# Performance work log

Measured on AMD Instinct MI355X. Metric: run time of the kernel, lower is better.

## Reference

```python
import jax, jax.numpy as jnp
import numpy as np

B, C, H, W = 16, 256, 64, 64
K = 1024


def setup_inputs() -> dict:
    key = jax.random.key(0)
    k1, k2 = jax.random.split(key)
    z = jax.random.normal(k1, (B, C, H, W), dtype=jnp.float32)
    codebook = jax.random.normal(k2, (K, C), dtype=jnp.float32)
    return {"z": z, "codebook": codebook}


def reference(z, codebook):
    # assign: nearest-code indices via squared euclidean distance
    b, c, h, w = z.shape
    zf = jnp.transpose(z, (0, 2, 3, 1)).reshape(-1, c)            # [N, C]
    # ||z||^2 - 2 z.cb^T + ||cb||^2  -> [N, K]
    dists = (jnp.sum(zf * zf, axis=1, keepdims=True)
             - 2.0 * jnp.einsum('nc,kc->nk', zf, codebook)
             + jnp.sum(codebook * codebook, axis=1)[None, :])
    idx = jnp.argmin(dists, axis=1)                                # [N]
    indices = idx.reshape(b, 1, h, w)                              # [B,1,H,W]
    # embed_code: gather codebook rows, back to BCHW
    zq = codebook[idx].reshape(b, h, w, c)                         # [B,H,W,C]
    zq = jnp.transpose(zq, (0, 3, 1, 2))                           # [B,C,H,W]
    return zq, indices
```

## Files before the change

kernel.cpp:

```cpp
#include <hip/hip_runtime.h>


#define HWSZ 4096
#define CDIM 256
#define KCODES 1024
#define NPIX 65536
#define ZQ_ELEMS (16 * 256 * 4096)
#define MARGIN 0.75f

#define WS_CBSWZ 0
#define WS_CBN64 524288
#define WS_CBN32 532480
#define WS_CNT   536576
#define WS_LISTS 536592

#define L_NRM    65536
#define L_MK     69632
#define L_SBEST  72704
#define L_FLP    73216
#define L_FLQ    73728
#define L_LCNT   74240
#define L_TOTAL  74496

typedef __attribute__((ext_vector_type(8))) short bf16x8;
typedef __attribute__((ext_vector_type(4))) float f32x4;
typedef __attribute__((ext_vector_type(4))) unsigned short us4;

#define MFMA16(a, b, c) __builtin_amdgcn_mfma_f32_16x16x32_bf16(a, b, c, 0, 0, 0)

__device__ __forceinline__ unsigned short f2bf(float f) {
  unsigned u = __float_as_uint(f);
  unsigned r = u + 0x7FFFu + ((u >> 16) & 1u);
  return (unsigned short)(r >> 16);
}

__device__ __forceinline__ unsigned cvtpk(float lo, float hi) {
  unsigned r;
  asm("v_cvt_pk_bf16_f32 %0, %1, %2" : "=v"(r) : "v"(lo), "v"(hi));
  return r;
}

__device__ __forceinline__ void gload_lds16(const void* g, void* l) {
  __builtin_amdgcn_global_load_lds(
      (const __attribute__((address_space(1))) unsigned int*)g,
      (__attribute__((address_space(3))) unsigned int*)l, 16, 0, 0);
}

__device__ __forceinline__ void ins3(unsigned& k1, unsigned& k2, unsigned& k3,
                                     unsigned k) {
  unsigned nk2, nk3;
  asm("v_med3_u32 %0, %1, %2, %3" : "=v"(nk2) : "v"(k1), "v"(k2), "v"(k));
  asm("v_med3_u32 %0, %1, %2, %3" : "=v"(nk3) : "v"(k2), "v"(k3), "v"(k));
  k1 = k1 < k ? k1 : k;
  k2 = nk2;
  k3 = nk3;
}

__device__ __forceinline__ float keyf(unsigned k) {
  return __uint_as_float(k & 0xFFFFFC00u);
}

__global__ void vq_prep(const float* __restrict__ cb,
                        unsigned short* __restrict__ cbswz,
                        double* __restrict__ cbn64,
                        float* __restrict__ cbn32p,
                        int* __restrict__ cnt) {
  const int t = threadIdx.x;
  if (blockIdx.x == 0 && t == 0) { cnt[0] = 0; cnt[1] = 0; }
  const int code = blockIdx.x * 4 + (t >> 6);
  const int lane = t & 63;
  const int c4 = lane * 4;

  float4 v = *(const float4*)(cb + (size_t)code * CDIM + c4);
  us4 hv;
  hv.x = f2bf(-2.f * v.x); hv.y = f2bf(-2.f * v.y);
  hv.z = f2bf(-2.f * v.z); hv.w = f2bf(-2.f * v.w);
  const int K = (code >> 9) * 32 + ((code >> 4) & 31);
  const int kk = c4 >> 5;
  const int lg = (c4 >> 3) & 3;
  const int within = (c4 & 7) * 2;
  size_t off = (size_t)K * 8192 + kk * 1024 + lg * 256 + (code & 15) * 16 + within;
  *(us4*)((char*)cbswz + off) = hv;

  double s = (double)v.x * v.x;
  s = fma((double)v.y, (double)v.y, s);
  s = fma((double)v.z, (double)v.z, s);
  s = fma((double)v.w, (double)v.w, s);
#pragma unroll
  for (int o = 32; o; o >>= 1) s += __shfl_xor(s, o, 64);
  if (lane == 0) {
    cbn64[code] = s;
    cbn32p[code] = (float)s + 512.0f;
  }
}

__launch_bounds__(256, 2)
__global__ void vq_stage1(const float* __restrict__ z,
                          const float* __restrict__ cb,
                          const unsigned short* __restrict__ cbswz,
                          const float* __restrict__ cbn32p,
                          float* __restrict__ out_zq,
                          float* __restrict__ out_idx,
                          int* __restrict__ cnt,
                          int* __restrict__ listA, int capA,
                          int* __restrict__ listB, int capB,
                          float* __restrict__ zws, int zcap) {
  extern __shared__ char smem[];
  const int t = threadIdx.x;
  const int w = t >> 6;
  const int lane = t & 63;
  const int lg = lane >> 4;
  const int lcode = lane & 15;
  const int h = w >> 1;
  const int q = w & 1;
  const int p0 = blockIdx.x * 128;
  const int b = p0 >> 12;
  const int hw0 = p0 & (HWSZ - 1);
  const float* zb = z + (size_t)b * (CDIM * HWSZ) + hw0;

  char* const wbuf = smem + w * 16384;
  char* const wb0 = wbuf;
  char* const wb1 = wbuf + 8192;
  float* nrm = (float*)(smem + L_NRM);

  const char* cbbase = (const char*)cbswz + (size_t)q * 262144 + lane * 16;

#define STAGE(CIDX, DST)                                              \
  {                                                                   \
    const char* gs_ = cbbase + ((size_t)(CIDX) << 13);                \
    gload_lds16(gs_,        (DST));                                   \
    gload_lds16(gs_ + 1024, (DST) + 1024);                            \
    gload_lds16(gs_ + 2048, (DST) + 2048);                            \
    gload_lds16(gs_ + 3072, (DST) + 3072);                            \
    gload_lds16(gs_ + 4096, (DST) + 4096);                            \
    gload_lds16(gs_ + 5120, (DST) + 5120);                            \
    gload_lds16(gs_ + 6144, (DST) + 6144);                            \
    gload_lds16(gs_ + 7168, (DST) + 7168);                            \
  }

  STAGE(0, wb0);
  STAGE(1, wb1);

  bf16x8 af[4][8];
#pragma unroll
  for (int T = 0; T < 4; ++T) {
    const float* zr = zb + (h * 64 + T * 16 + lcode);
#pragma unroll
    for (int kk = 0; kk < 8; ++kk) {
      const int ch0 = kk * 32 + lg * 8;
      float v0 = zr[(size_t)(ch0 + 0) * HWSZ];
      float v1 = zr[(size_t)(ch0 + 1) * HWSZ];
      float v2 = zr[(size_t)(ch0 + 2) * HWSZ];
      float v3 = zr[(size_t)(ch0 + 3) * HWSZ];
      float v4 = zr[(size_t)(ch0 + 4) * HWSZ];
      float v5 = zr[(size_t)(ch0 + 5) * HWSZ];
      float v6 = zr[(size_t)(ch0 + 6) * HWSZ];
      float v7 = zr[(size_t)(ch0 + 7) * HWSZ];
      unsigned p01 = cvtpk(v0, v1);
      unsigned p23 = cvtpk(v2, v3);
      unsigned p45 = cvtpk(v4, v5);
      unsigned p67 = cvtpk(v6, v7);
      bf16x8 f;
      f[0] = (short)(p01 & 0xFFFF); f[1] = (short)(p01 >> 16);
      f[2] = (short)(p23 & 0xFFFF); f[3] = (short)(p23 >> 16);
      f[4] = (short)(p45 & 0xFFFF); f[5] = (short)(p45 >> 16);
      f[6] = (short)(p67 & 0xFFFF); f[7] = (short)(p67 >> 16);
      af[T][kk] = f;
    }
  }

  *(float4*)(nrm + t * 4) = *(const float4*)(cbn32p + t * 4);
  __syncthreads();

  unsigned k1[4][4], k2[4][4], k3[4][4];
#pragma unroll
  for (int T = 0; T < 4; ++T)
#pragma unroll
    for (int q4 = 0; q4 < 4; ++q4) {
      k1[T][q4] = 0xFFFFFFFFu; k2[T][q4] = 0xFFFFFFFFu; k3[T][q4] = 0xFFFFFFFFu;
    }

  const int lane16 = lane * 16;
  const float* nrmp = nrm + q * 512 + lcode;
  const int kbase = q * 512 + lcode;
  float cnn = nrmp[0];

#define BODY(CIDX, RBUF, DOSTAGE, WN)                                 \
  {                                                                   \
    asm volatile("s_waitcnt vmcnt(" WN ")" ::: "memory");             \
    const float cn_ = cnn;                                            \
    if ((CIDX) < 31) cnn = nrmp[((CIDX) + 1) * 16];                   \
    const char* pb_ = (RBUF) + lane16;                                \
    f32x4 a0 = {cn_, cn_, cn_, cn_};                                  \
    f32x4 a1 = {cn_, cn_, cn_, cn_};                                  \
    f32x4 a2 = {cn_, cn_, cn_, cn_};                                  \
    f32x4 a3 = {cn_, cn_, cn_, cn_};                                  \
    _Pragma("unroll")                                                 \
    for (int kk = 0; kk < 8; ++kk) {                                  \
      bf16x8 bf_ = *(const bf16x8*)(pb_ + kk * 1024);                 \
      a0 = MFMA16(af[0][kk], bf_, a0);                                \
      a1 = MFMA16(af[1][kk], bf_, a1);                                \
      a2 = MFMA16(af[2][kk], bf_, a2);                                \
      a3 = MFMA16(af[3][kk], bf_, a3);                                \
    }                                                                 \
    asm volatile("s_waitcnt lgkmcnt(0)" ::: "memory");                \
    __builtin_amdgcn_sched_barrier(0);                                \
    if (DOSTAGE) STAGE((CIDX) + 2, RBUF);                             \
    const unsigned code_ = (unsigned)(kbase + (CIDX) * 16);           \
    _Pragma("unroll")                                                 \
    for (int q4 = 0; q4 < 4; ++q4) {                                  \
      ins3(k1[0][q4], k2[0][q4], k3[0][q4],                           \
           (__float_as_uint(a0[q4]) & 0xFFFFFC00u) | code_);          \
      ins3(k1[1][q4], k2[1][q4], k3[1][q4],                           \
           (__float_as_uint(a1[q4]) & 0xFFFFFC00u) | code_);          \
      ins3(k1[2][q4], k2[2][q4], k3[2][q4],                           \
           (__float_as_uint(a2[q4]) & 0xFFFFFC00u) | code_);          \
      ins3(k1[3][q4], k2[3][q4], k3[3][q4],                           \
           (__float_as_uint(a3[q4]) & 0xFFFFFC00u) | code_);          \
    }                                                                 \
  }

#pragma unroll 1
  for (int c2 = 0; c2 < 30; c2 += 2) {
    BODY(c2 + 0, wb0, 1, "8");
    BODY(c2 + 1, wb1, 1, "8");
  }
  BODY(30, wb0, 0, "8");
  BODY(31, wb1, 0, "0");
#undef BODY
#undef STAGE

#pragma unroll
  for (int mask = 1; mask <= 8; mask <<= 1) {
#pragma unroll
    for (int T = 0; T < 4; ++T)
#pragma unroll
      for (int q4 = 0; q4 < 4; ++q4) {
        unsigned o1 = __shfl_xor(k1[T][q4], mask, 64);
        unsigned o2 = __shfl_xor(k2[T][q4], mask, 64);
        unsigned o3 = __shfl_xor(k3[T][q4], mask, 64);
        ins3(k1[T][q4], k2[T][q4], k3[T][q4], o1);
        ins3(k1[T][q4], k2[T][q4], k3[T][q4], o2);
        ins3(k1[T][q4], k2[T][q4], k3[T][q4], o3);
      }
  }

  unsigned* mk = (unsigned*)(smem + L_MK);
  int* sbest = (int*)(smem + L_SBEST);
  int* flp = (int*)(smem + L_FLP);
  int* flq = (int*)(smem + L_FLQ);
  int* lcnt = (int*)(smem + L_LCNT);
  if (t == 0) *lcnt = 0;
  if (lcode == 0) {
#pragma unroll
    for (int T = 0; T < 4; ++T)
#pragma unroll
      for (int q4 = 0; q4 < 4; ++q4) {
        int row = h * 64 + T * 16 + lg * 4 + q4;
        unsigned* d = mk + (row * 2 + q) * 3;
        d[0] = k1[T][q4]; d[1] = k2[T][q4]; d[2] = k3[T][q4];
      }
  }
  __syncthreads();

  if (t < 128) {
    unsigned a1 = mk[t * 6 + 0], a2 = mk[t * 6 + 1], a3 = mk[t * 6 + 2];
    ins3(a1, a2, a3, mk[t * 6 + 3]);
    ins3(a1, a2, a3, mk[t * 6 + 4]);
    ins3(a1, a2, a3, mk[t * 6 + 5]);
    const int p = p0 + t;
    const int i1 = (int)(a1 & 1023u);
    sbest[t] = i1;
    out_idx[p] = (float)i1;
    float f1 = keyf(a1);
    float g2 = keyf(a2) - f1;
    float g3 = keyf(a3) - f1;
    if (g3 < MARGIN) {
      int pos = atomicAdd(cnt + 1, 1);
      if (pos < capB) listB[pos] = p;
    } else if (g2 < MARGIN) {
      int pos = atomicAdd(cnt, 1);
      if (pos < capA) {
        listA[2 * pos] = p | (i1 << 16);
        listA[2 * pos + 1] = (int)(a2 & 1023u) | ((int)(a3 & 1023u) << 16);
        if (pos < zcap) {
          int li = atomicAdd(lcnt, 1);
          flp[li] = p;
          flq[li] = pos;
        }
      }
    }
  }
  __syncthreads();

  {
    const int px = t & 127;
    const int best = sbest[px];
    const int ch0g = (t >> 7) * 128;
    const float* crow = cb + (size_t)best * CDIM + ch0g;
    float* ob = out_zq + (size_t)b * (CDIM * HWSZ) + (size_t)ch0g * HWSZ + hw0 + px;
#pragma unroll 4
    for (int c2 = 0; c2 < 128; c2 += 4) {
      float4 v = *(const float4*)(crow + c2);
      ob[(size_t)(c2 + 0) * HWSZ] = v.x;
      ob[(size_t)(c2 + 1) * HWSZ] = v.y;
      ob[(size_t)(c2 + 2) * HWSZ] = v.z;
      ob[(size_t)(c2 + 3) * HWSZ] = v.w;
    }
  }

  {
    const int nf = *lcnt;
    for (int e = 0; e < nf; ++e) {
      const int p = flp[e];
      const int slot = flq[e];
      const int bb = p >> 12;
      const int hh = p & (HWSZ - 1);
      zws[(size_t)slot * 256 + t] =
          z[(size_t)bb * (CDIM * HWSZ) + (size_t)t * HWSZ + hh];
    }
  }
}

__launch_bounds__(256)
__global__ void vq_fix(const float* __restrict__ z,
                       const float* __restrict__ cb,
                       const double* __restrict__ cbn64,
                       float* __restrict__ out_zq,
                       float* __restrict__ out_idx,
                       const int* __restrict__ cnt,
                       const int* __restrict__ listA, int capA,
                       const float* __restrict__ zws, int zcap,
                       const int* __restrict__ listB, int capB) {
  const int t = threadIdx.x;
  const int w = t >> 6;
  const int lane = t & 63;

  {
    const int wid = blockIdx.x * 4 + w;
    const int nw = gridDim.x * 4;
    int n = cnt[0];
    if (n > capA) n = capA;

    for (int i = wid; i < n; i += nw) {
      const int e0 = listA[2 * i];
      const int e1 = listA[2 * i + 1];
      const int p = e0 & 0xFFFF;
      int cand[3];
      cand[0] = (e0 >> 16) & 1023;
      cand[1] = e1 & 0xFFFF;
      cand[2] = (e1 >> 16) & 1023;
      const int b = p >> 12;
      const int hw = p & (HWSZ - 1);
      const int ch0 = lane * 4;

      double zv[4];
      if (i < zcap) {
        float4 zf = ((const float4*)(zws + (size_t)i * 256))[lane];
        zv[0] = (double)zf.x; zv[1] = (double)zf.y;
        zv[2] = (double)zf.z; zv[3] = (double)zf.w;
      } else {
        const float* zb = z + (size_t)b * (CDIM * HWSZ) + hw;
#pragma unroll
        for (int j = 0; j < 4; ++j) zv[j] = (double)zb[(size_t)(ch0 + j) * HWSZ];
      }

      double d[3];
#pragma unroll
      for (int tt = 0; tt < 3; ++tt) {
        float4 cv = *(const float4*)(cb + (size_t)cand[tt] * CDIM + ch0);
        double s = zv[0] * (double)cv.x;
        s = fma(zv[1], (double)cv.y, s);
        s = fma(zv[2], (double)cv.z, s);
        s = fma(zv[3], (double)cv.w, s);
#pragma unroll
        for (int off = 32; off; off >>= 1) s += __shfl_xor(s, off, 64);
        d[tt] = fma(-2.0, s, cbn64[cand[tt]]);
      }

      double bd = d[0];
      int bi = cand[0];
#pragma unroll
      for (int tt = 1; tt < 3; ++tt) {
        bool takes = (d[tt] < bd) || (d[tt] == bd && cand[tt] < bi);
        bd = takes ? d[tt] : bd;
        bi = takes ? cand[tt] : bi;
      }

      if (bi != cand[0]) {
        if (lane == 0) out_idx[p] = (float)bi;
        float4 cv = *(const float4*)(cb + (size_t)bi * CDIM + ch0);
        float* ob = out_zq + (size_t)b * (CDIM * HWSZ) + hw;
        ob[(size_t)(ch0 + 0) * HWSZ] = cv.x;
        ob[(size_t)(ch0 + 1) * HWSZ] = cv.y;
        ob[(size_t)(ch0 + 2) * HWSZ] = cv.z;
        ob[(size_t)(ch0 + 3) * HWSZ] = cv.w;
      }
    }
  }

  __shared__ double zl[256];
  __shared__ double sd[4];
  __shared__ int si[4];
  __shared__ int sfin;
  int n = cnt[1];
  if (n > capB) n = capB;

  for (int i = blockIdx.x; i < n; i += gridDim.x) {
    const int p = listB[i];
    const int b = p >> 12;
    const int hw = p & (HWSZ - 1);
    const float* zb = z + (size_t)b * (CDIM * HWSZ) + hw;
    zl[t] = (double)zb[(size_t)t * HWSZ];
    __syncthreads();

    const int g = t >> 2;
    const int sub = t & 3;
    const double* zq4 = zl + sub * 64;
    double bd = 1e300;
    int bi = 0;

    for (int j = 0; j < 16; ++j) {
      const int code = g + 64 * j;
      const float* crow = cb + (size_t)code * CDIM + sub * 64;
      double s = 0.0;
#pragma unroll
      for (int q4 = 0; q4 < 64; q4 += 4) {
        float4 cv = *(const float4*)(crow + q4);
        s = fma(zq4[q4 + 0], (double)cv.x, s);
        s = fma(zq4[q4 + 1], (double)cv.y, s);
        s = fma(zq4[q4 + 2], (double)cv.z, s);
        s = fma(zq4[q4 + 3], (double)cv.w, s);
      }
      s += __shfl_xor(s, 1, 64);
      s += __shfl_xor(s, 2, 64);
      double d = fma(-2.0, s, cbn64[code]);
      bool takes = (d < bd) || (d == bd && code < bi);
      bd = takes ? d : bd;
      bi = takes ? code : bi;
    }

#pragma unroll
    for (int off = 4; off <= 32; off <<= 1) {
      double od = __shfl_xor(bd, off, 64);
      int oi = __shfl_xor(bi, off, 64);
      bool takes = (od < bd) || (od == bd && oi < bi);
      bd = takes ? od : bd;
      bi = takes ? oi : bi;
    }
    if (lane == 0) { sd[w] = bd; si[w] = bi; }
    __syncthreads();
    if (t == 0) {
      double fd = sd[0];
      int fi = si[0];
#pragma unroll
      for (int k = 1; k < 4; ++k) {
        bool takes = (sd[k] < fd) || (sd[k] == fd && si[k] < fi);
        fd = takes ? sd[k] : fd;
        fi = takes ? si[k] : fi;
      }
      const int old = (int)out_idx[p];
      sfin = (fi != old) ? fi : -1;
      if (fi != old) out_idx[p] = (float)fi;
    }
    __syncthreads();
    const int best = sfin;
    if (best >= 0) {
      float* ob = out_zq + (size_t)b * (CDIM * HWSZ) + hw;
      ob[(size_t)t * HWSZ] = cb[(size_t)best * CDIM + t];
    }
    __syncthreads();
  }
}

extern "C" void kernel_launch(void* const* d_in, const int* in_sizes, int n_in,
                              void* d_out, int out_size, void* d_ws, size_t ws_size,
                              hipStream_t stream) {
  const float* z = (const float*)d_in[0];
  const float* cb = (const float*)d_in[1];
  float* out = (float*)d_out;
  float* out_zq = out;
  float* out_idx = out + ZQ_ELEMS;

  char* ws = (char*)d_ws;
  unsigned short* cbswz = (unsigned short*)(ws + WS_CBSWZ);
  double* cbn64 = (double*)(ws + WS_CBN64);
  float* cbn32p = (float*)(ws + WS_CBN32);
  int* cnt = (int*)(ws + WS_CNT);

  long long avail = (long long)ws_size - WS_LISTS;
  if (avail < 0) avail = 0;
  long long capA_ll = (avail / 4) / 8;
  if (capA_ll > NPIX) capA_ll = NPIX;
  int capA = (int)capA_ll;
  int* listA = (int*)(ws + WS_LISTS);
  long long rem = avail - (long long)capA * 8;
  long long capB_ll = rem / 8;
  if (capB_ll > NPIX) capB_ll = NPIX;
  if (capB_ll < 0) capB_ll = 0;
  int capB = (int)capB_ll;
  int* listB = (int*)(ws + WS_LISTS + (size_t)capA * 8);
  long long zoff = (WS_LISTS + (long long)capA * 8 + (long long)capB * 4 + 15) &
                   ~15LL;
  long long zcap_ll = ((long long)ws_size - zoff) / 1024;
  if (zcap_ll < 0) zcap_ll = 0;
  if (zcap_ll > capA) zcap_ll = capA;
  int zcap = (int)zcap_ll;
  float* zws = (float*)(ws + zoff);

  hipFuncSetAttribute(reinterpret_cast<const void*>(vq_stage1),
                      hipFuncAttributeMaxDynamicSharedMemorySize, L_TOTAL);

  vq_prep<<<256, 256, 0, stream>>>(cb, cbswz, cbn64, cbn32p, cnt);
  vq_stage1<<<512, 256, L_TOTAL, stream>>>(z, cb, cbswz, cbn32p, out_zq, out_idx,
                                           cnt, listA, capA, listB, capB,
                                           zws, zcap);
  vq_fix<<<256, 256, 0, stream>>>(z, cb, cbn64, out_zq, out_idx,
                                  cnt, listA, capA, zws, zcap, listB, capB);
}
```

Baseline: 154.8 us.

## Give each wave all codes for 64 pixels and overlap top-3 insert with MFMA

```diff
diff --git a/kernel.cpp b/kernel.cpp
--- a/kernel.cpp
+++ b/kernel.cpp
@@ -15,12 +15,11 @@
 #define WS_LISTS 536592
 
 #define L_NRM    65536
-#define L_MK     69632
-#define L_SBEST  72704
-#define L_FLP    73216
-#define L_FLQ    73728
-#define L_LCNT   74240
-#define L_TOTAL  74496
+#define L_SBEST  69632
+#define L_FLP    70656
+#define L_FLQ    71680
+#define L_LCNT   72704
+#define L_TOTAL  72832
 
 typedef __attribute__((ext_vector_type(8))) short bf16x8;
 typedef __attribute__((ext_vector_type(4))) float f32x4;
@@ -75,7 +74,7 @@
   us4 hv;
   hv.x = f2bf(-2.f * v.x); hv.y = f2bf(-2.f * v.y);
   hv.z = f2bf(-2.f * v.z); hv.w = f2bf(-2.f * v.w);
-  const int K = (code >> 9) * 32 + ((code >> 4) & 31);
+  const int K = code >> 4;
   const int kk = c4 >> 5;
   const int lg = (c4 >> 3) & 3;
   const int within = (c4 & 7) * 2;
@@ -94,7 +93,7 @@
   }
 }
 
-__launch_bounds__(256, 2)
+__launch_bounds__(256)
 __global__ void vq_stage1(const float* __restrict__ z,
                           const float* __restrict__ cb,
                           const unsigned short* __restrict__ cbswz,
@@ -111,19 +110,16 @@
   const int lane = t & 63;
   const int lg = lane >> 4;
   const int lcode = lane & 15;
-  const int h = w >> 1;
-  const int q = w & 1;
-  const int p0 = blockIdx.x * 128;
+  const int p0 = blockIdx.x * 256;
   const int b = p0 >> 12;
   const int hw0 = p0 & (HWSZ - 1);
   const float* zb = z + (size_t)b * (CDIM * HWSZ) + hw0;
 
-  char* const wbuf = smem + w * 16384;
-  char* const wb0 = wbuf;
-  char* const wb1 = wbuf + 8192;
+  char* const wb0 = smem + w * 16384;
+  char* const wb1 = smem + w * 16384 + 8192;
   float* nrm = (float*)(smem + L_NRM);
 
-  const char* cbbase = (const char*)cbswz + (size_t)q * 262144 + lane * 16;
+  const char* cbbase = (const char*)cbswz + lane * 16;
 
 #define STAGE(CIDX, DST)                                              \
   {                                                                   \
@@ -144,7 +140,7 @@
   bf16x8 af[4][8];
 #pragma unroll
   for (int T = 0; T < 4; ++T) {
-    const float* zr = zb + (h * 64 + T * 16 + lcode);
+    const float* zr = zb + (w * 64 + T * 16 + lcode);
 #pragma unroll
     for (int kk = 0; kk < 8; ++kk) {
       const int ch0 = kk * 32 + lg * 8;
@@ -181,53 +177,64 @@
     }
 
   const int lane16 = lane * 16;
-  const float* nrmp = nrm + q * 512 + lcode;
-  const int kbase = q * 512 + lcode;
+  const float* nrmp = nrm + lcode;
   float cnn = nrmp[0];
 
-#define BODY(CIDX, RBUF, DOSTAGE, WN)                                 \
+  f32x4 aA0, aA1, aA2, aA3, aB0, aB1, aB2, aB3;
+
+#define MM(CIDX, RBUF, AN, DOSTAGE, WN)                               \
   {                                                                   \
     asm volatile("s_waitcnt vmcnt(" WN ")" ::: "memory");             \
     const float cn_ = cnn;                                            \
-    if ((CIDX) < 31) cnn = nrmp[((CIDX) + 1) * 16];                   \
+    if ((CIDX) < 63) cnn = nrmp[((CIDX) + 1) * 16];                   \
     const char* pb_ = (RBUF) + lane16;                                \
-    f32x4 a0 = {cn_, cn_, cn_, cn_};                                  \
-    f32x4 a1 = {cn_, cn_, cn_, cn_};                                  \
-    f32x4 a2 = {cn_, cn_, cn_, cn_};                                  \
-    f32x4 a3 = {cn_, cn_, cn_, cn_};                                  \
+    AN##0 = (f32x4){cn_, cn_, cn_, cn_};                              \
+    AN##1 = (f32x4){cn_, cn_, cn_, cn_};                              \
+    AN##2 = (f32x4){cn_, cn_, cn_, cn_};                              \
+    AN##3 = (f32x4){cn_, cn_, cn_, cn_};                              \
     _Pragma("unroll")                                                 \
     for (int kk = 0; kk < 8; ++kk) {                                  \
       bf16x8 bf_ = *(const bf16x8*)(pb_ + kk * 1024);                 \
-      a0 = MFMA16(af[0][kk], bf_, a0);                                \
-      a1 = MFMA16(af[1][kk], bf_, a1);                                \
-      a2 = MFMA16(af[2][kk], bf_, a2);                                \
-      a3 = MFMA16(af[3][kk], bf_, a3);                                \
+      AN##0 = MFMA16(af[0][kk], bf_, AN##0);                          \
+      AN##1 = MFMA16(af[1][kk], bf_, AN##1);                          \
+      AN##2 = MFMA16(af[2][kk], bf_, AN##2);                          \
+      AN##3 = MFMA16(af[3][kk], bf_, AN##3);                          \
     }                                                                 \
     asm volatile("s_waitcnt lgkmcnt(0)" ::: "memory");                \
     __builtin_amdgcn_sched_barrier(0);                                \
     if (DOSTAGE) STAGE((CIDX) + 2, RBUF);                             \
-    const unsigned code_ = (unsigned)(kbase + (CIDX) * 16);           \
+  }
+
+#define INS(CODEC, AO)                                                \
+  {                                                                   \
+    const unsigned code_ = (unsigned)((CODEC) * 16 + lcode);          \
     _Pragma("unroll")                                                 \
     for (int q4 = 0; q4 < 4; ++q4) {                                  \
       ins3(k1[0][q4], k2[0][q4], k3[0][q4],                           \
-           (__float_as_uint(a0[q4]) & 0xFFFFFC00u) | code_);          \
+           (__float_as_uint(AO##0[q4]) & 0xFFFFFC00u) | code_);       \
       ins3(k1[1][q4], k2[1][q4], k3[1][q4],                           \
-           (__float_as_uint(a1[q4]) & 0xFFFFFC00u) | code_);          \
+           (__float_as_uint(AO##1[q4]) & 0xFFFFFC00u) | code_);       \
       ins3(k1[2][q4], k2[2][q4], k3[2][q4],                           \
-           (__float_as_uint(a2[q4]) & 0xFFFFFC00u) | code_);          \
+           (__float_as_uint(AO##2[q4]) & 0xFFFFFC00u) | code_);       \
       ins3(k1[3][q4], k2[3][q4], k3[3][q4],                           \
-           (__float_as_uint(a3[q4]) & 0xFFFFFC00u) | code_);          \
+           (__float_as_uint(AO##3[q4]) & 0xFFFFFC00u) | code_);       \
     }                                                                 \
   }
 
+  MM(0, wb0, aA, 1, "8")
+  MM(1, wb1, aB, 1, "8") INS(0, aA)
 #pragma unroll 1
-  for (int c2 = 0; c2 < 30; c2 += 2) {
-    BODY(c2 + 0, wb0, 1, "8");
-    BODY(c2 + 1, wb1, 1, "8");
-  }
-  BODY(30, wb0, 0, "8");
-  BODY(31, wb1, 0, "0");
-#undef BODY
+  for (int c2 = 2; c2 <= 58; c2 += 2) {
+    MM(c2 + 0, wb0, aA, 1, "8") INS(c2 - 1, aB)
+    MM(c2 + 1, wb1, aB, 1, "8") INS(c2 + 0, aA)
+  }
+  MM(60, wb0, aA, 1, "8") INS(59, aB)
+  MM(61, wb1, aB, 1, "8") INS(60, aA)
+  MM(62, wb0, aA, 0, "8") INS(61, aB)
+  MM(63, wb1, aB, 0, "0") INS(62, aA)
+  INS(63, aB)
+#undef MM
+#undef INS
 #undef STAGE
 
 #pragma unroll
@@ -245,62 +252,52 @@
       }
   }
 
-  unsigned* mk = (unsigned*)(smem + L_MK);
   int* sbest = (int*)(smem + L_SBEST);
   int* flp = (int*)(smem + L_FLP);
   int* flq = (int*)(smem + L_FLQ);
   int* lcnt = (int*)(smem + L_LCNT);
   if (t == 0) *lcnt = 0;
+  __syncthreads();
+
   if (lcode == 0) {
 #pragma unroll
     for (int T = 0; T < 4; ++T)
 #pragma unroll
       for (int q4 = 0; q4 < 4; ++q4) {
-        int row = h * 64 + T * 16 + lg * 4 + q4;
-        unsigned* d = mk + (row * 2 + q) * 3;
-        d[0] = k1[T][q4]; d[1] = k2[T][q4]; d[2] = k3[T][q4];
+        const int row = w * 64 + T * 16 + lg * 4 + q4;
+        const int p = p0 + row;
+        const unsigned a1 = k1[T][q4], a2 = k2[T][q4], a3 = k3[T][q4];
+        const int i1 = (int)(a1 & 1023u);
+        sbest[row] = i1;
+        out_idx[p] = (float)i1;
+        float f1 = keyf(a1);
+        float g2 = keyf(a2) - f1;
+        float g3 = keyf(a3) - f1;
+        if (g3 < MARGIN) {
+          int pos = atomicAdd(cnt + 1, 1);
+          if (pos < capB) listB[pos] = p;
+        } else if (g2 < MARGIN) {
+          int pos = atomicAdd(cnt, 1);
+          if (pos < capA) {
+            listA[2 * pos] = p | (i1 << 16);
+            listA[2 * pos + 1] = (int)(a2 & 1023u) | ((int)(a3 & 1023u) << 16);
+            if (pos < zcap) {
+              int li = atomicAdd(lcnt, 1);
+              flp[li] = p;
+              flq[li] = pos;
+            }
+          }
+        }
       }
   }
   __syncthreads();
 
-  if (t < 128) {
-    unsigned a1 = mk[t * 6 + 0], a2 = mk[t * 6 + 1], a3 = mk[t * 6 + 2];
-    ins3(a1, a2, a3, mk[t * 6 + 3]);
-    ins3(a1, a2, a3, mk[t * 6 + 4]);
-    ins3(a1, a2, a3, mk[t * 6 + 5]);
-    const int p = p0 + t;
-    const int i1 = (int)(a1 & 1023u);
-    sbest[t] = i1;
-    out_idx[p] = (float)i1;
-    float f1 = keyf(a1);
-    float g2 = keyf(a2) - f1;
-    float g3 = keyf(a3) - f1;
-    if (g3 < MARGIN) {
-      int pos = atomicAdd(cnt + 1, 1);
-      if (pos < capB) listB[pos] = p;
-    } else if (g2 < MARGIN) {
-      int pos = atomicAdd(cnt, 1);
-      if (pos < capA) {
-        listA[2 * pos] = p | (i1 << 16);
-        listA[2 * pos + 1] = (int)(a2 & 1023u) | ((int)(a3 & 1023u) << 16);
-        if (pos < zcap) {
-          int li = atomicAdd(lcnt, 1);
-          flp[li] = p;
-          flq[li] = pos;
-        }
-      }
-    }
-  }
-  __syncthreads();
-
   {
-    const int px = t & 127;
-    const int best = sbest[px];
-    const int ch0g = (t >> 7) * 128;
-    const float* crow = cb + (size_t)best * CDIM + ch0g;
-    float* ob = out_zq + (size_t)b * (CDIM * HWSZ) + (size_t)ch0g * HWSZ + hw0 + px;
+    const int best = sbest[t];
+    const float* crow = cb + (size_t)best * CDIM;
+    float* ob = out_zq + (size_t)b * (CDIM * HWSZ) + hw0 + t;
 #pragma unroll 4
-    for (int c2 = 0; c2 < 128; c2 += 4) {
+    for (int c2 = 0; c2 < 256; c2 += 4) {
       float4 v = *(const float4*)(crow + c2);
       ob[(size_t)(c2 + 0) * HWSZ] = v.x;
       ob[(size_t)(c2 + 1) * HWSZ] = v.y;
@@ -512,7 +509,7 @@
                       hipFuncAttributeMaxDynamicSharedMemorySize, L_TOTAL);
 
   vq_prep<<<256, 256, 0, stream>>>(cb, cbswz, cbn64, cbn32p, cnt);
-  vq_stage1<<<512, 256, L_TOTAL, stream>>>(z, cb, cbswz, cbn32p, out_zq, out_idx,
+  vq_stage1<<<256, 256, L_TOTAL, stream>>>(z, cb, cbswz, cbn32p, out_zq, out_idx,
                                            cnt, listA, capA, listB, capB,
                                            zws, zcap);
   vq_fix<<<256, 256, 0, stream>>>(z, cb, cbn64, out_zq, out_idx,
```

After: 198.2 us. +28.0%, slower.
